# Kernel tuning notes

Hardware: AMD Instinct MI355X
Metric: run time of the kernel (lower is better)

The kernel has to match this reference:

```python
import jax, jax.numpy as jnp
import numpy as np

B, S = 8, 1024          # sequences, tokens per sequence (batched prefill)
DIM = 2048
N_HEADS, N_KV_HEADS = 16, 8
HEAD_DIM = DIM // N_HEADS   # 128
N_REP = N_HEADS // N_KV_HEADS
BLOCK_SIZE = 16
NUM_BLOCKS = B * S // BLOCK_SIZE  # 512
T = B * S
ROPE_THETA = 10000.0


def apply_rotary_paged(x, positions):
    # x: [T, H, head_dim], positions: [T] int -- Llama-style interleaved rotary
    hd = x.shape[-1]
    inv_freq = 1.0 / (ROPE_THETA ** (jnp.arange(0, hd, 2, dtype=jnp.float32) / hd))  # [hd/2]
    ang = positions.astype(jnp.float32)[:, None] * inv_freq[None, :]                  # [T, hd/2]
    cos = jnp.cos(ang)[:, None, :]  # [T, 1, hd/2]
    sin = jnp.sin(ang)[:, None, :]
    xr, xi = x[..., 0::2], x[..., 1::2]
    out_r = xr * cos - xi * sin
    out_i = xr * sin + xi * cos
    return jnp.stack([out_r, out_i], axis=-1).reshape(x.shape).astype(x.dtype)


def setup_inputs() -> dict:
    key = jax.random.key(0)
    ks = jax.random.split(key, 6)
    std = 0.02
    x = jax.random.normal(ks[0], (T, DIM), dtype=jnp.float32)
    wq = jax.random.normal(ks[1], (DIM, N_HEADS * HEAD_DIM), dtype=jnp.float32) * std
    wk = jax.random.normal(ks[2], (DIM, N_KV_HEADS * HEAD_DIM), dtype=jnp.float32) * std
    wv = jax.random.normal(ks[3], (DIM, N_KV_HEADS * HEAD_DIM), dtype=jnp.float32) * std
    wo = jax.random.normal(ks[4], (N_HEADS * HEAD_DIM, DIM), dtype=jnp.float32) * std
    k_cache = jnp.zeros((NUM_BLOCKS, 1, N_KV_HEADS, BLOCK_SIZE, HEAD_DIM), dtype=jnp.float32)
    v_cache = jnp.zeros((NUM_BLOCKS, 1, N_KV_HEADS, BLOCK_SIZE, HEAD_DIM), dtype=jnp.float32)
    positions = jnp.tile(jnp.arange(S, dtype=jnp.int32), B)          # [T]
    tokens_per_seq = jnp.full((B,), S, dtype=jnp.int32)
    context_lengths = jnp.full((B,), S, dtype=jnp.int32)
    block_tables = jnp.arange(NUM_BLOCKS, dtype=jnp.int32).reshape(B, S // BLOCK_SIZE)
    return {"x": x, "wq": wq, "wk": wk, "wv": wv, "wo": wo,
            "k_cache": k_cache, "v_cache": v_cache,
            "positions": positions, "tokens_per_seq": tokens_per_seq,
            "context_lengths": context_lengths, "block_tables": block_tables,
            "layer_idx": 0}


def reference(x, wq, wk, wv, wo, k_cache, v_cache,
              positions, tokens_per_seq, context_lengths, block_tables, layer_idx):
    # QKV projections (Linear, no bias)
    xq = (x @ wq).reshape(T, N_HEADS, HEAD_DIM)
    xk = (x @ wk).reshape(T, N_KV_HEADS, HEAD_DIM)
    xv = (x @ wv).reshape(T, N_KV_HEADS, HEAD_DIM)
    xq = apply_rotary_paged(xq, positions)
    xk = apply_rotary_paged(xk, positions)

    # --- scatter new K/V into paged caches via block tables ---
    seq_ids = jnp.arange(T, dtype=jnp.int32) // S                 # [T]
    blk = block_tables[seq_ids, positions // BLOCK_SIZE]           # [T]
    off = positions % BLOCK_SIZE                                   # [T]
    k_cache = k_cache.at[blk, layer_idx, :, off, :].set(xk)        # [T,kvh,hd]
    v_cache = v_cache.at[blk, layer_idx, :, off, :].set(xv)

    # --- gather full K/V per sequence from the paged caches ---
    kpos = jnp.arange(S, dtype=jnp.int32)                          # [S]
    blk_g = block_tables[:, kpos // BLOCK_SIZE]                    # [B, S]
    off_g = jnp.broadcast_to(kpos % BLOCK_SIZE, (B, S))            # [B, S]
    gk = k_cache[blk_g, layer_idx, :, off_g, :]                    # [B, S, kvh, hd]
    gv = v_cache[blk_g, layer_idx, :, off_g, :]

    # GQA: repeat_interleave kv heads to n_heads
    gk = jnp.repeat(gk, N_REP, axis=2)                             # [B, S, h, hd]
    gv = jnp.repeat(gv, N_REP, axis=2)

    q = xq.reshape(B, S, N_HEADS, HEAD_DIM)
    scale = 1.0 / np.sqrt(HEAD_DIM).astype(np.float32)
    scores = jnp.einsum('bqhd,bkhd->bhqk', q, gk) * scale          # [B,h,S,S]

    # causal mask using token positions (prefill)
    q_pos = positions.reshape(B, S)
    mask = q_pos[:, None, :, None] < kpos[None, None, None, :]     # [B,1,S,S]
    scores = jnp.where(mask, -jnp.inf, scores)

    probs = jax.nn.softmax(scores.astype(jnp.float32), axis=-1).astype(q.dtype)
    attn = jnp.einsum('bhqk,bkhd->bqhd', probs, gv)                # [B,S,h,hd]
    out = attn.reshape(T, N_HEADS * HEAD_DIM) @ wo                 # resid dropout = identity (eval)
    return out
```

## Files before the change

kernel.cpp:

```cpp
#include <hip/hip_runtime.h>
#include <stdint.h>

#define TTOK  8192
#define DIMM  2048
#define NH    16
#define NKV   8
#define HD    128
#define SEQ   1024
#define BATCH 8
#define BLKSZ 16

typedef unsigned short u16;
typedef __attribute__((ext_vector_type(8))) short bfrag;
typedef __attribute__((ext_vector_type(4))) float f32x4;

__device__ __forceinline__ float bf2f(u16 u) {
  unsigned int v = ((unsigned int)u) << 16;
  float f; __builtin_memcpy(&f, &v, 4); return f;
}
__device__ __forceinline__ u16 f2bf(float f) {
  unsigned int v; __builtin_memcpy(&v, &f, 4);
  v = v + 0x7FFFu + ((v >> 16) & 1u);
  return (u16)(v >> 16);
}

__device__ __forceinline__ void gll16(const void* g, void* l) {
  __builtin_amdgcn_global_load_lds(
      (__attribute__((address_space(1))) void*)(g),
      (__attribute__((address_space(3))) void*)(l), 16, 0, 0);
}
__device__ __forceinline__ void hard_fence() {
  asm volatile("" ::: "memory");
  __builtin_amdgcn_s_waitcnt(0);
  asm volatile("" ::: "memory");
}

__global__ __launch_bounds__(256) void f32_to_bf16(const float* __restrict__ in,
                                                   u16* __restrict__ out, size_t n) {
  size_t i = ((size_t)blockIdx.x * 256 + threadIdx.x) * 8;
  if (i >= n) return;
  float4 a = *(const float4*)(in + i);
  float4 b = *(const float4*)(in + i + 4);
  union { u16 o[8]; uint4 v; } u;
  u.o[0] = f2bf(a.x); u.o[1] = f2bf(a.y); u.o[2] = f2bf(a.z); u.o[3] = f2bf(a.w);
  u.o[4] = f2bf(b.x); u.o[5] = f2bf(b.y); u.o[6] = f2bf(b.z); u.o[7] = f2bf(b.w);
  *(uint4*)(out + i) = u.v;
}

__global__ __launch_bounds__(256) void ktranspose_f(const float* __restrict__ in,
                                                    u16* __restrict__ out, int K, int N) {
  __shared__ __align__(16) u16 tile[64 * 65];
  int n0 = blockIdx.x * 64, k0 = blockIdx.y * 64;
  int tx = threadIdx.x & 63, ty = threadIdx.x >> 6;
  for (int r = 0; r < 16; ++r) {
    int kk = r * 4 + ty;
    tile[kk * 65 + tx] = f2bf(in[(size_t)(k0 + kk) * N + n0 + tx]);
  }
  __syncthreads();
  for (int r = 0; r < 16; ++r) {
    int nn = r * 4 + ty;
    out[(size_t)(n0 + nn) * K + k0 + tx] = tile[tx * 65 + nn];
  }
}

template <typename OutT>
__global__ __launch_bounds__(256) void gemm_bt(const u16* __restrict__ A,
                                               const u16* __restrict__ Bt,
                                               OutT* __restrict__ C,
                                               int M, int N, int K) {
  __shared__ __align__(16) u16 As[128 * 32];
  __shared__ __align__(16) u16 Bs[128 * 32];
  int tid = threadIdx.x;
  int wave = tid >> 6, lane = tid & 63, quad = lane >> 4, l15 = lane & 15;
  int m0 = blockIdx.y * 128, n0 = blockIdx.x * 128;
  int wm = (wave >> 1) * 64, wn = (wave & 1) * 64;

  f32x4 acc[4][4];
  for (int i = 0; i < 4; ++i)
    for (int j = 0; j < 4; ++j) acc[i][j] = (f32x4){0.f, 0.f, 0.f, 0.f};

  int g0 = wave * 64 + lane;
  int g1 = 256 + wave * 64 + lane;
  const u16* Arow0 = A + (size_t)(m0 + (g0 >> 2)) * K + (g0 & 3) * 8;
  const u16* Arow1 = A + (size_t)(m0 + (g1 >> 2)) * K + (g1 & 3) * 8;
  const u16* Brow0 = Bt + (size_t)(n0 + (g0 >> 2)) * K + (g0 & 3) * 8;
  const u16* Brow1 = Bt + (size_t)(n0 + (g1 >> 2)) * K + (g1 & 3) * 8;
  char* AsB = (char*)As;
  char* BsB = (char*)Bs;
  int lds0 = wave * 1024, lds1 = 4096 + wave * 1024;

  for (int k0 = 0; k0 < K; k0 += 32) {
    __syncthreads();
    asm volatile("" ::: "memory");
    gll16(Arow0 + k0, AsB + lds0);
    gll16(Arow1 + k0, AsB + lds1);
    gll16(Brow0 + k0, BsB + lds0);
    gll16(Brow1 + k0, BsB + lds1);
    hard_fence();
    __syncthreads();

    bfrag af[4], bfv[4];
    for (int im = 0; im < 4; ++im) {
      int m = wm + im * 16 + l15;
      af[im] = *(const bfrag*)(AsB + m * 64 + quad * 16);
    }
    for (int jn = 0; jn < 4; ++jn) {
      int n = wn + jn * 16 + l15;
      bfv[jn] = *(const bfrag*)(BsB + n * 64 + quad * 16);
    }
    for (int im = 0; im < 4; ++im)
      for (int jn = 0; jn < 4; ++jn)
        acc[im][jn] = __builtin_amdgcn_mfma_f32_16x16x32_bf16(af[im], bfv[jn], acc[im][jn], 0, 0, 0);
  }

  for (int im = 0; im < 4; ++im)
    for (int jn = 0; jn < 4; ++jn)
      for (int r = 0; r < 4; ++r) {
        int row = m0 + wm + im * 16 + quad * 4 + r;
        int col = n0 + wn + jn * 16 + l15;
        if constexpr (__is_same(OutT, float))
          C[(size_t)row * N + col] = acc[im][jn][r];
        else
          C[(size_t)row * N + col] = f2bf(acc[im][jn][r]);
      }
}

__global__ __launch_bounds__(256) void rope_scatter(const u16* __restrict__ xqkv,
                                                    const int* __restrict__ positions,
                                                    const int* __restrict__ btab,
                                                    u16* __restrict__ qb,
                                                    u16* __restrict__ kb,
                                                    u16* __restrict__ vbuf) {
  int t = blockIdx.x;
  int tid = threadIdx.x;
  int b = t >> 10, srow = t & 1023;
  int pos = positions[t];
  int blk = btab[b * (SEQ / BLKSZ) + (pos >> 4)];
  int off = pos & (BLKSZ - 1);
  int c0 = tid * 16;

  struct __align__(16) { uint4 a, bq; } vv, oo;
  const u16* src = xqkv + (size_t)t * 4096 + c0;
  vv.a  = *(const uint4*)src;
  vv.bq = *(const uint4*)(src + 8);
  const u16* v = (const u16*)&vv;
  u16* o = (u16*)&oo;

  if (c0 < 3072) {
    int dbase = c0 & 127;
    float fpos = (float)pos;
    for (int j = 0; j < 8; ++j) {
      int i = (dbase >> 1) + j;
      float inv = exp2f(-(float)i * (13.287712379549449f / 64.0f));
      float ang = fpos * inv;
      float sn, cs;
      sincosf(ang, &sn, &cs);
      float fr = bf2f(v[2 * j]), fi = bf2f(v[2 * j + 1]);
      o[2 * j]     = f2bf(fr * cs - fi * sn);
      o[2 * j + 1] = f2bf(fr * sn + fi * cs);
    }
  } else {
    for (int j = 0; j < 16; ++j) o[j] = v[j];
  }

  u16* dst;
  if (c0 < 2048) {
    int head = c0 >> 7, d0 = c0 & 127;
    dst = qb + (((size_t)(b * NH + head)) * SEQ + srow) * HD + d0;
  } else if (c0 < 3072) {
    int cc = c0 - 2048;
    int kvh = cc >> 7, d0 = cc & 127;
    dst = kb + (((size_t)(blk * NKV + kvh) * BLKSZ + off)) * HD + d0;
  } else {
    int cc = c0 - 3072;
    int kvh = cc >> 7, d0 = cc & 127;
    dst = vbuf + (((size_t)(blk * NKV + kvh) * BLKSZ + off)) * HD + d0;
  }
  *(uint4*)dst = oo.a;
  *(uint4*)(dst + 8) = oo.bq;
}

#define KVT 64
#define KS_STRIDE 272
#define VT_STRIDE 144
#define PS_STRIDE 144

__global__ __launch_bounds__(512) void attn_kernel(const u16* __restrict__ Q,
                                                   const u16* __restrict__ Kc,
                                                   const u16* __restrict__ Vc,
                                                   const int* __restrict__ positions,
                                                   const int* __restrict__ btab,
                                                   u16* __restrict__ O) {
  __shared__ __align__(16) u16 Ks[KVT * (KS_STRIDE / 2)];
  __shared__ __align__(16) u16 Vt[HD * (VT_STRIDE / 2)];
  __shared__ __align__(16) u16 Ps[8 * 16 * (PS_STRIDE / 2)];
  const float SM_SCALE = 0.08838834764831845f;
  const float LOG2E    = 1.4426950408889634f;
  const float C1       = SM_SCALE * LOG2E;
  const float NEGBIG   = -30000.0f;
  const float NEGINIT  = -1e30f;
  const float DEFER2   = 8.0f * LOG2E;

  int tid = threadIdx.x;
  int wave = tid >> 6, lane = tid & 63, quad = lane >> 4, l15 = lane & 15;
  int bid = blockIdx.x;
  int bh = bid >> 2, pr = bid & 3;
  int b = bh >> 4, h = bh & 15, kvh = h >> 1;
  const int* btrow = btab + b * (SEQ / BLKSZ);

  char* KsB = (char*)Ks;
  char* VtB = (char*)Vt;
  char* myPsB = (char*)Ps + wave * 16 * PS_STRIDE;

  int tokA = tid >> 4;
  int tokB = tokA + 32;
  int dgK  = tid & 15;
  int tokV = (tid & 31) * 2;
  int vd0  = (tid >> 5) * 8;

  uint4 kr0, kr1, vr0, vr1;

  auto load_tile = [&](int kti) {
    int i0 = kti >> 4;
    int b0 = btrow[i0], b1 = btrow[i0 + 1], b2 = btrow[i0 + 2], b3 = btrow[i0 + 3];
    const u16* KA = Kc + ((size_t)(((tokA < 16) ? b0 : b1) * NKV + kvh) * BLKSZ + (tokA & 15)) * HD + dgK * 8;
    const u16* KB = Kc + ((size_t)(((tokB < 48) ? b2 : b3) * NKV + kvh) * BLKSZ + (tokB & 15)) * HD + dgK * 8;
    kr0 = *(const uint4*)KA;
    kr1 = *(const uint4*)KB;
    int bv = (tokV < 16) ? b0 : (tokV < 32) ? b1 : (tokV < 48) ? b2 : b3;
    const u16* VA = Vc + ((size_t)(bv * NKV + kvh) * BLKSZ + (tokV & 15)) * HD + vd0;
    vr0 = *(const uint4*)VA;
    vr1 = *(const uint4*)(VA + HD);
  };

  for (int pass = 0; pass < 2; ++pass) {
    int yt = pass ? (7 - pr) : pr;
    int q0 = yt * 128;
    int qw = q0 + wave * 16;

    const u16* Qbase = Q + ((size_t)bh * SEQ + qw) * HD;

    bfrag aq[4];
#pragma unroll
    for (int kb2 = 0; kb2 < 4; ++kb2)
      aq[kb2] = *(const bfrag*)(Qbase + (size_t)l15 * HD + kb2 * 32 + quad * 8);

    int qpos[4];
#pragma unroll
    for (int r = 0; r < 4; ++r)
      qpos[r] = positions[(size_t)b * SEQ + qw + quad * 4 + r];

    f32x4 oa[8];
#pragma unroll
    for (int jd = 0; jd < 8; ++jd) oa[jd] = (f32x4){0.f, 0.f, 0.f, 0.f};
    float m2_i[4], l_i[4];
#pragma unroll
    for (int r = 0; r < 4; ++r) { m2_i[r] = NEGINIT; l_i[r] = 0.f; }

    int kend = q0 + 128;
    load_tile(0);

    for (int kt = 0; kt < kend; kt += KVT) {
      __syncthreads();
      *(uint4*)(KsB + tokA * KS_STRIDE + dgK * 16) = kr0;
      *(uint4*)(KsB + tokB * KS_STRIDE + dgK * 16) = kr1;
      {
        const u16* p0 = (const u16*)&vr0;
        const u16* p1 = (const u16*)&vr1;
#pragma unroll
        for (int jj = 0; jj < 8; ++jj) {
          unsigned int val = (unsigned int)p0[jj] | ((unsigned int)p1[jj] << 16);
          *(unsigned int*)(VtB + (vd0 + jj) * VT_STRIDE + tokV * 2) = val;
        }
      }
      __syncthreads();

      if (kt + KVT < kend) load_tile(kt + KVT);

      if (kt <= qw + 15) {
        f32x4 sa[4];
#pragma unroll
        for (int jn = 0; jn < 4; ++jn) sa[jn] = (f32x4){0.f, 0.f, 0.f, 0.f};
#pragma unroll
        for (int kb2 = 0; kb2 < 4; ++kb2) {
#pragma unroll
          for (int jn = 0; jn < 4; ++jn) {
            bfrag bk = *(const bfrag*)(KsB + (jn * 16 + l15) * KS_STRIDE + (kb2 * 4 + quad) * 16);
            sa[jn] = __builtin_amdgcn_mfma_f32_16x16x32_bf16(aq[kb2], bk, sa[jn], 0, 0, 0);
          }
        }

        float m2x[4];
#pragma unroll
        for (int r = 0; r < 4; ++r) {
#pragma unroll
          for (int jn = 0; jn < 4; ++jn) {
            float s = sa[jn][r];
            if (kt + jn * 16 + l15 > qpos[r]) s = NEGBIG;
            sa[jn][r] = s;
          }
          float m0 = fmaxf(fmaxf(sa[0][r], sa[1][r]), fmaxf(sa[2][r], sa[3][r]));
          m0 = fmaxf(m0, __shfl_xor(m0, 1, 64));
          m0 = fmaxf(m0, __shfl_xor(m0, 2, 64));
          m0 = fmaxf(m0, __shfl_xor(m0, 4, 64));
          m0 = fmaxf(m0, __shfl_xor(m0, 8, 64));
          m2x[r] = m0 * C1;
        }

        bool ok = (m2x[0] <= m2_i[0] + DEFER2) && (m2x[1] <= m2_i[1] + DEFER2) &&
                  (m2x[2] <= m2_i[2] + DEFER2) && (m2x[3] <= m2_i[3] + DEFER2);
        if (__all(ok)) {
#pragma unroll
          for (int r = 0; r < 4; ++r) {
            float rs = 0.f;
#pragma unroll
            for (int jn = 0; jn < 4; ++jn) {
              float pv = exp2f(sa[jn][r] * C1 - m2_i[r]);
              sa[jn][r] = pv;
              rs += pv;
            }
            rs += __shfl_xor(rs, 1, 64);
            rs += __shfl_xor(rs, 2, 64);
            rs += __shfl_xor(rs, 4, 64);
            rs += __shfl_xor(rs, 8, 64);
            l_i[r] += rs;
          }
        } else {
          float alpha[4];
#pragma unroll
          for (int r = 0; r < 4; ++r) {
            float m2n = fmaxf(m2_i[r], m2x[r]);
            float al = exp2f(m2_i[r] - m2n);
            float rs = 0.f;
#pragma unroll
            for (int jn = 0; jn < 4; ++jn) {
              float pv = exp2f(sa[jn][r] * C1 - m2n);
              sa[jn][r] = pv;
              rs += pv;
            }
            rs += __shfl_xor(rs, 1, 64);
            rs += __shfl_xor(rs, 2, 64);
            rs += __shfl_xor(rs, 4, 64);
            rs += __shfl_xor(rs, 8, 64);
            l_i[r] = l_i[r] * al + rs;
            m2_i[r] = m2n;
            alpha[r] = al;
          }
#pragma unroll
          for (int jd = 0; jd < 8; ++jd) {
            oa[jd][0] *= alpha[0];
            oa[jd][1] *= alpha[1];
            oa[jd][2] *= alpha[2];
            oa[jd][3] *= alpha[3];
          }
        }

#pragma unroll
        for (int r = 0; r < 4; ++r) {
          int q = quad * 4 + r;
#pragma unroll
          for (int jn = 0; jn < 4; ++jn)
            *(u16*)(myPsB + q * PS_STRIDE + (jn * 16 + l15) * 2) = f2bf(sa[jn][r]);
        }
        bfrag ap0 = *(const bfrag*)(myPsB + l15 * PS_STRIDE + quad * 16);
        bfrag ap1 = *(const bfrag*)(myPsB + l15 * PS_STRIDE + 64 + quad * 16);
#pragma unroll
        for (int jd = 0; jd < 8; ++jd) {
          int d = jd * 16 + l15;
          bfrag bv0 = *(const bfrag*)(VtB + d * VT_STRIDE + quad * 16);
          bfrag bv1 = *(const bfrag*)(VtB + d * VT_STRIDE + 64 + quad * 16);
          oa[jd] = __builtin_amdgcn_mfma_f32_16x16x32_bf16(ap0, bv0, oa[jd], 0, 0, 0);
          oa[jd] = __builtin_amdgcn_mfma_f32_16x16x32_bf16(ap1, bv1, oa[jd], 0, 0, 0);
        }
      }
    }

#pragma unroll
    for (int r = 0; r < 4; ++r) {
      float inv = 1.0f / fmaxf(l_i[r], 1e-30f);
      size_t trow = (size_t)b * SEQ + qw + quad * 4 + r;
#pragma unroll
      for (int jd = 0; jd < 8; ++jd)
        O[trow * 2048 + (size_t)h * HD + jd * 16 + l15] = f2bf(oa[jd][r] * inv);
    }
  }
}

extern "C" void kernel_launch(void* const* d_in, const int* in_sizes, int n_in,
                              void* d_out, int out_size, void* d_ws, size_t ws_size,
                              hipStream_t stream) {
  (void)in_sizes; (void)n_in; (void)out_size;
  const float* xf  = (const float*)d_in[0];
  const float* wqf = (const float*)d_in[1];
  const float* wkf = (const float*)d_in[2];
  const float* wvf = (const float*)d_in[3];
  const float* wof = (const float*)d_in[4];
  const int* positions = (const int*)d_in[7];
  const int* btab      = (const int*)d_in[10];
  float* out = (float*)d_out;

  u16* ws    = (u16*)d_ws;
  u16* woT   = ws;
  u16* wqkvT = woT + (size_t)2048 * 2048;
  u16* xbf   = wqkvT + (size_t)4096 * 2048;
  u16* xqkv  = xbf + (size_t)8192 * 2048;
  u16* qb    = xqkv + (size_t)8192 * 4096;
  u16* kbuf  = qb + (size_t)8192 * 2048;
  u16* vbuf  = kbuf + (size_t)8192 * 1024;
  u16* wsend = vbuf + (size_t)8192 * 1024;

  size_t base_elems = (size_t)(wsend - ws);
  size_t obuf_elems = (size_t)8192 * 2048;
  u16* obuf;
  if (ws_size >= (base_elems + obuf_elems) * sizeof(u16))
    obuf = wsend;
  else
    obuf = wqkvT;

  if (ws_size < base_elems * sizeof(u16)) return;

  f32_to_bf16<<<dim3(8192), 256, 0, stream>>>(xf, xbf, (size_t)8192 * 2048);
  ktranspose_f<<<dim3(32, 32), 256, 0, stream>>>(wqf, wqkvT, 2048, 2048);
  ktranspose_f<<<dim3(16, 32), 256, 0, stream>>>(wkf, wqkvT + (size_t)2048 * 2048, 2048, 1024);
  ktranspose_f<<<dim3(16, 32), 256, 0, stream>>>(wvf, wqkvT + (size_t)3072 * 2048, 2048, 1024);
  ktranspose_f<<<dim3(32, 32), 256, 0, stream>>>(wof, woT, 2048, 2048);
  gemm_bt<u16><<<dim3(32, 64), 256, 0, stream>>>(xbf, wqkvT, xqkv, 8192, 4096, 2048);
  rope_scatter<<<dim3(8192), 256, 0, stream>>>(xqkv, positions, btab, qb, kbuf, vbuf);
  attn_kernel<<<dim3(512), 512, 0, stream>>>(qb, kbuf, vbuf, positions, btab, obuf);
  gemm_bt<float><<<dim3(16, 64), 256, 0, stream>>>(obuf, woT, out, 8192, 2048, 2048);
}
```

Measured before the change: 621.2 us.

## Replace GEMM with 256x256-tile double-buffered 8-wave kernel with swizzled LDS

```diff
diff --git a/kernel.cpp b/kernel.cpp
--- a/kernel.cpp
+++ b/kernel.cpp
@@ -29,10 +29,11 @@
       (__attribute__((address_space(1))) void*)(g),
       (__attribute__((address_space(3))) void*)(l), 16, 0, 0);
 }
-__device__ __forceinline__ void hard_fence() {
-  asm volatile("" ::: "memory");
-  __builtin_amdgcn_s_waitcnt(0);
-  asm volatile("" ::: "memory");
+
+__device__ __forceinline__ void lds_barrier() {
+  asm volatile("s_waitcnt lgkmcnt(0)" ::: "memory");
+  __builtin_amdgcn_sched_barrier(0);
+  __builtin_amdgcn_s_barrier();
 }
 
 __global__ __launch_bounds__(256) void f32_to_bf16(const float* __restrict__ in,
@@ -64,65 +65,164 @@
 }
 
 template <typename OutT>
-__global__ __launch_bounds__(256) void gemm_bt(const u16* __restrict__ A,
-                                               const u16* __restrict__ Bt,
-                                               OutT* __restrict__ C,
-                                               int M, int N, int K) {
-  __shared__ __align__(16) u16 As[128 * 32];
-  __shared__ __align__(16) u16 Bs[128 * 32];
+__global__ __launch_bounds__(512, 2) void gemm_bt8(const u16* __restrict__ A,
+                                                   const u16* __restrict__ Bt,
+                                                   OutT* __restrict__ C,
+                                                   int M, int N, int K) {
+  __shared__ __align__(16) u16 AS[2][256 * 64];
+  __shared__ __align__(16) u16 BS[2][256 * 64];
+  (void)M;
   int tid = threadIdx.x;
-  int wave = tid >> 6, lane = tid & 63, quad = lane >> 4, l15 = lane & 15;
-  int m0 = blockIdx.y * 128, n0 = blockIdx.x * 128;
-  int wm = (wave >> 1) * 64, wn = (wave & 1) * 64;
-
-  f32x4 acc[4][4];
-  for (int i = 0; i < 4; ++i)
-    for (int j = 0; j < 4; ++j) acc[i][j] = (f32x4){0.f, 0.f, 0.f, 0.f};
-
-  int g0 = wave * 64 + lane;
-  int g1 = 256 + wave * 64 + lane;
-  const u16* Arow0 = A + (size_t)(m0 + (g0 >> 2)) * K + (g0 & 3) * 8;
-  const u16* Arow1 = A + (size_t)(m0 + (g1 >> 2)) * K + (g1 & 3) * 8;
-  const u16* Brow0 = Bt + (size_t)(n0 + (g0 >> 2)) * K + (g0 & 3) * 8;
-  const u16* Brow1 = Bt + (size_t)(n0 + (g1 >> 2)) * K + (g1 & 3) * 8;
-  char* AsB = (char*)As;
-  char* BsB = (char*)Bs;
-  int lds0 = wave * 1024, lds1 = 4096 + wave * 1024;
-
-  for (int k0 = 0; k0 < K; k0 += 32) {
-    __syncthreads();
-    asm volatile("" ::: "memory");
-    gll16(Arow0 + k0, AsB + lds0);
-    gll16(Arow1 + k0, AsB + lds1);
-    gll16(Brow0 + k0, BsB + lds0);
-    gll16(Brow1 + k0, BsB + lds1);
-    hard_fence();
-    __syncthreads();
-
-    bfrag af[4], bfv[4];
-    for (int im = 0; im < 4; ++im) {
-      int m = wm + im * 16 + l15;
-      af[im] = *(const bfrag*)(AsB + m * 64 + quad * 16);
-    }
-    for (int jn = 0; jn < 4; ++jn) {
-      int n = wn + jn * 16 + l15;
-      bfv[jn] = *(const bfrag*)(BsB + n * 64 + quad * 16);
-    }
-    for (int im = 0; im < 4; ++im)
-      for (int jn = 0; jn < 4; ++jn)
-        acc[im][jn] = __builtin_amdgcn_mfma_f32_16x16x32_bf16(af[im], bfv[jn], acc[im][jn], 0, 0, 0);
-  }
-
-  for (int im = 0; im < 4; ++im)
-    for (int jn = 0; jn < 4; ++jn)
-      for (int r = 0; r < 4; ++r) {
-        int row = m0 + wm + im * 16 + quad * 4 + r;
-        int col = n0 + wn + jn * 16 + l15;
-        if constexpr (__is_same(OutT, float))
-          C[(size_t)row * N + col] = acc[im][jn][r];
-        else
-          C[(size_t)row * N + col] = f2bf(acc[im][jn][r]);
-      }
+  int w = tid >> 6, lane = tid & 63, quad = lane >> 4, l15 = lane & 15;
+  int wr = w >> 2, wc = w & 3;
+
+  int nwg = gridDim.x * gridDim.y;
+  int id = blockIdx.y * gridDim.x + blockIdx.x;
+  int swz = (id & 7) * (nwg >> 3) + (id >> 3);
+  int bx = swz % gridDim.x, by = swz / gridDim.x;
+  int m0 = by * 256, n0 = bx * 256;
+
+  size_t Kb = (size_t)K * 2;
+  int nt = K >> 6;
+
+  int s_lr = lane >> 3;
+  int s_lo = ((lane & 7) ^ s_lr) * 16;
+  auto stageA = [&](int half, int tk, char* As) {
+    int rloc = half * 128 + w * 16;
+    const char* src = (const char*)A + (size_t)(m0 + rloc + s_lr) * Kb + (size_t)tk * 128 + s_lo;
+    char* dst = As + rloc * 128 + lane * 16;
+    gll16(src, dst);
+    gll16(src + 8 * Kb, dst + 1024);
+  };
+  auto stageB = [&](int half, int tk, char* Bs) {
+    int rloc = half * 128 + w * 16;
+    const char* src = (const char*)Bt + (size_t)(n0 + rloc + s_lr) * Kb + (size_t)tk * 128 + s_lo;
+    char* dst = Bs + rloc * 128 + lane * 16;
+    gll16(src, dst);
+    gll16(src + 8 * Kb, dst + 1024);
+  };
+
+  f32x4 acc[2][4][2][2];
+#pragma unroll
+  for (int mh = 0; mh < 2; ++mh)
+#pragma unroll
+    for (int f = 0; f < 4; ++f)
+#pragma unroll
+      for (int nh = 0; nh < 2; ++nh)
+#pragma unroll
+        for (int g = 0; g < 2; ++g) acc[mh][f][nh][g] = (f32x4){0.f, 0.f, 0.f, 0.f};
+
+  stageA(0, 0, (char*)AS[0]); stageA(1, 0, (char*)AS[0]);
+  stageB(0, 0, (char*)BS[0]); stageB(1, 0, (char*)BS[0]);
+  if (nt > 1) {
+    stageA(0, 1, (char*)AS[1]); stageA(1, 1, (char*)AS[1]);
+    stageB(0, 1, (char*)BS[1]); stageB(1, 1, (char*)BS[1]);
+    asm volatile("s_waitcnt vmcnt(8)" ::: "memory");
+  } else {
+    asm volatile("s_waitcnt vmcnt(0)" ::: "memory");
+  }
+  lds_barrier();
+
+  int rswz = (l15 & 7) << 4;
+  int aRow = wr * 64 + l15;
+  int bRow = wc * 32 + l15;
+
+  for (int t = 0; t < nt; ++t) {
+    char* As = (char*)AS[t & 1];
+    char* Bs = (char*)BS[t & 1];
+    bool pre = (t + 2 < nt);
+    bfrag aA[4][2], aB0[2][2], aB1[2][2];
+
+#pragma unroll
+    for (int f = 0; f < 4; ++f)
+#pragma unroll
+      for (int kk = 0; kk < 2; ++kk)
+        aA[f][kk] = *(const bfrag*)(As + (aRow + f * 16) * 128 + ((kk * 64 + quad * 16) ^ rswz));
+#pragma unroll
+    for (int g = 0; g < 2; ++g)
+#pragma unroll
+      for (int kk = 0; kk < 2; ++kk)
+        aB0[g][kk] = *(const bfrag*)(Bs + (bRow + g * 16) * 128 + ((kk * 64 + quad * 16) ^ rswz));
+    __builtin_amdgcn_s_setprio(1);
+#pragma unroll
+    for (int f = 0; f < 4; ++f)
+#pragma unroll
+      for (int g = 0; g < 2; ++g)
+#pragma unroll
+        for (int kk = 0; kk < 2; ++kk)
+          acc[0][f][0][g] = __builtin_amdgcn_mfma_f32_16x16x32_bf16(aA[f][kk], aB0[g][kk], acc[0][f][0][g], 0, 0, 0);
+    __builtin_amdgcn_s_setprio(0);
+    lds_barrier();
+
+    if (pre) { stageA(0, t + 2, As); stageB(0, t + 2, Bs); }
+#pragma unroll
+    for (int g = 0; g < 2; ++g)
+#pragma unroll
+      for (int kk = 0; kk < 2; ++kk)
+        aB1[g][kk] = *(const bfrag*)(Bs + (bRow + 128 + g * 16) * 128 + ((kk * 64 + quad * 16) ^ rswz));
+    __builtin_amdgcn_s_setprio(1);
+#pragma unroll
+    for (int f = 0; f < 4; ++f)
+#pragma unroll
+      for (int g = 0; g < 2; ++g)
+#pragma unroll
+        for (int kk = 0; kk < 2; ++kk)
+          acc[0][f][1][g] = __builtin_amdgcn_mfma_f32_16x16x32_bf16(aA[f][kk], aB1[g][kk], acc[0][f][1][g], 0, 0, 0);
+    __builtin_amdgcn_s_setprio(0);
+    lds_barrier();
+
+    if (pre) stageB(1, t + 2, Bs);
+#pragma unroll
+    for (int f = 0; f < 4; ++f)
+#pragma unroll
+      for (int kk = 0; kk < 2; ++kk)
+        aA[f][kk] = *(const bfrag*)(As + (aRow + 128 + f * 16) * 128 + ((kk * 64 + quad * 16) ^ rswz));
+    __builtin_amdgcn_s_setprio(1);
+#pragma unroll
+    for (int f = 0; f < 4; ++f)
+#pragma unroll
+      for (int g = 0; g < 2; ++g)
+#pragma unroll
+        for (int kk = 0; kk < 2; ++kk)
+          acc[1][f][1][g] = __builtin_amdgcn_mfma_f32_16x16x32_bf16(aA[f][kk], aB1[g][kk], acc[1][f][1][g], 0, 0, 0);
+    __builtin_amdgcn_s_setprio(0);
+    lds_barrier();
+
+    if (pre) stageA(1, t + 2, As);
+    __builtin_amdgcn_s_setprio(1);
+#pragma unroll
+    for (int f = 0; f < 4; ++f)
+#pragma unroll
+      for (int g = 0; g < 2; ++g)
+#pragma unroll
+        for (int kk = 0; kk < 2; ++kk)
+          acc[1][f][0][g] = __builtin_amdgcn_mfma_f32_16x16x32_bf16(aA[f][kk], aB0[g][kk], acc[1][f][0][g], 0, 0, 0);
+    __builtin_amdgcn_s_setprio(0);
+    if (pre)
+      asm volatile("s_waitcnt vmcnt(8)" ::: "memory");
+    else if (t + 1 < nt)
+      asm volatile("s_waitcnt vmcnt(0)" ::: "memory");
+    lds_barrier();
+  }
+
+#pragma unroll
+  for (int mh = 0; mh < 2; ++mh)
+#pragma unroll
+    for (int f = 0; f < 4; ++f)
+#pragma unroll
+      for (int nh = 0; nh < 2; ++nh)
+#pragma unroll
+        for (int g = 0; g < 2; ++g)
+#pragma unroll
+          for (int rr = 0; rr < 4; ++rr) {
+            int row = m0 + wr * 64 + mh * 128 + f * 16 + quad * 4 + rr;
+            int col = n0 + wc * 32 + nh * 128 + g * 16 + l15;
+            float v = acc[mh][f][nh][g][rr];
+            if constexpr (__is_same(OutT, float))
+              C[(size_t)row * N + col] = v;
+            else
+              C[(size_t)row * N + col] = f2bf(v);
+          }
 }
 
 __global__ __launch_bounds__(256) void rope_scatter(const u16* __restrict__ xqkv,
@@ -424,8 +524,8 @@
   ktranspose_f<<<dim3(16, 32), 256, 0, stream>>>(wkf, wqkvT + (size_t)2048 * 2048, 2048, 1024);
   ktranspose_f<<<dim3(16, 32), 256, 0, stream>>>(wvf, wqkvT + (size_t)3072 * 2048, 2048, 1024);
   ktranspose_f<<<dim3(32, 32), 256, 0, stream>>>(wof, woT, 2048, 2048);
-  gemm_bt<u16><<<dim3(32, 64), 256, 0, stream>>>(xbf, wqkvT, xqkv, 8192, 4096, 2048);
+  gemm_bt8<u16><<<dim3(16, 32), 512, 0, stream>>>(xbf, wqkvT, xqkv, 8192, 4096, 2048);
   rope_scatter<<<dim3(8192), 256, 0, stream>>>(xqkv, positions, btab, qb, kbuf, vbuf);
   attn_kernel<<<dim3(512), 512, 0, stream>>>(qb, kbuf, vbuf, positions, btab, obuf);
-  gemm_bt<float><<<dim3(16, 64), 256, 0, stream>>>(obuf, woT, out, 8192, 2048, 2048);
-}
+  gemm_bt8<float><<<dim3(8, 32), 512, 0, stream>>>(obuf, woT, out, 8192, 2048, 2048);
+}
```

Measured after the change: 560.9 us. 1.11x faster.
